# Performance work log

Measured on AMD Instinct MI355X. Metric: run time of the kernel, lower is better.

Reference implementation:

```python
import jax, jax.numpy as jnp
import numpy as np

B, S, TV, TT, E, H = 16, 8, 256, 64, 512, 512


def setup_inputs() -> dict:
    key = jax.random.key(0)
    ks = jax.random.split(key, 24)
    sc = 0.02
    p = lambda k, shape: jax.random.normal(k, shape, jnp.float32) * sc
    inp = {
        'vid_feats': jax.random.normal(ks[0], (B, S, TV, 2 * E), jnp.float32),
        'text_feats': jax.random.normal(ks[1], (B, S, TT, E), jnp.float32),
        'segment_labels': jax.random.randint(ks[2], (B, S), 0, 6),
        # bidirectional LSTM params for video encoder (input dim 2E)
        'vid_Wx_f': p(ks[3], (2 * E, 4 * H)), 'vid_Wh_f': p(ks[4], (H, 4 * H)), 'vid_b_f': jnp.zeros((4 * H,), jnp.float32),
        'vid_Wx_b': p(ks[5], (2 * E, 4 * H)), 'vid_Wh_b': p(ks[6], (H, 4 * H)), 'vid_b_b': jnp.zeros((4 * H,), jnp.float32),
        # bidirectional LSTM params for text encoder (input dim E)
        'txt_Wx_f': p(ks[7], (E, 4 * H)), 'txt_Wh_f': p(ks[8], (H, 4 * H)), 'txt_b_f': jnp.zeros((4 * H,), jnp.float32),
        'txt_Wx_b': p(ks[9], (E, 4 * H)), 'txt_Wh_b': p(ks[10], (H, 4 * H)), 'txt_b_b': jnp.zeros((4 * H,), jnp.float32),
        # state_query MLP: Linear(4H,H) -> ReLU -> (Dropout eval) -> Linear(H,1)
        'sq_W1': p(ks[11], (4 * H, H)), 'sq_b1': jnp.zeros((H,), jnp.float32),
        'sq_W2': p(ks[12], (H, 1)), 'sq_b2': jnp.zeros((1,), jnp.float32),
        # relation_query MLP
        'rq_W1': p(ks[13], (4 * H, H)), 'rq_b1': jnp.zeros((H,), jnp.float32),
        'rq_W2': p(ks[14], (H, 1)), 'rq_b2': jnp.zeros((1,), jnp.float32),
    }
    return inp


def _lstm_last(x, Wx, Wh, b):
    # x: [N, T, D] -> last hidden state [N, H]; gate order i,f,g,o (torch convention)
    xg = jnp.einsum('ntd,dg->ntg', x, Wx) + b  # precompute input projections
    h0 = jnp.zeros((x.shape[0], Wh.shape[0]), x.dtype)

    def step(carry, xt):
        h, c = carry
        i, f, g, o = jnp.split(xt + h @ Wh, 4, axis=-1)
        c = jax.nn.sigmoid(f) * c + jax.nn.sigmoid(i) * jnp.tanh(g)
        h = jax.nn.sigmoid(o) * jnp.tanh(c)
        return (h, c), None

    (h, _), _ = jax.lax.scan(step, (h0, h0), jnp.swapaxes(xg, 0, 1))
    return h


def _bilstm(x, Wxf, Whf, bf, Wxb, Whb, bb):
    # final hidden of fwd dir + final hidden of bwd dir (run on reversed seq)
    hf = _lstm_last(x, Wxf, Whf, bf)
    hb = _lstm_last(x[:, ::-1], Wxb, Whb, bb)
    return jnp.concatenate([hf, hb], axis=-1)  # [N, 2H]


def reference(vid_feats, text_feats,
              vid_Wx_f, vid_Wh_f, vid_b_f, vid_Wx_b, vid_Wh_b, vid_b_b,
              txt_Wx_f, txt_Wh_f, txt_b_f, txt_Wx_b, txt_Wh_b, txt_b_b,
              sq_W1, sq_b1, sq_W2, sq_b2, rq_W1, rq_b1, rq_W2, rq_b2,
              segment_labels):
    b, s = vid_feats.shape[0], vid_feats.shape[1]
    vh = _bilstm(vid_feats.reshape(b * s, vid_feats.shape[2], vid_feats.shape[3]),
                 vid_Wx_f, vid_Wh_f, vid_b_f, vid_Wx_b, vid_Wh_b, vid_b_b)  # [B*S, 2H]
    th = _bilstm(text_feats.reshape(b * s, text_feats.shape[2], text_feats.shape[3]),
                 txt_Wx_f, txt_Wh_f, txt_b_f, txt_Wx_b, txt_Wh_b, txt_b_b)  # [B*S, 2H]
    feats = jnp.concatenate([vh, th], axis=-1).reshape(b, s, -1)  # [B, S, 4H]

    def mlp(W1, b1, W2, b2):
        h = jax.nn.relu(feats @ W1 + b1)  # Dropout is identity in eval mode
        return (h @ W2 + b2)[..., 0]      # [B, S]

    state_score = mlp(sq_W1, sq_b1, sq_W2, sq_b2)
    rel_score = mlp(rq_W1, rq_b1, rq_W2, rq_b2)
    # labels <= 3 -> state_query, labels in {4,5} -> relation_query
    sel = jnp.where(segment_labels <= 3, state_score, rel_score)  # [B, S]
    return jax.nn.sigmoid(sel.mean(axis=1))  # [B]
```

## Files before the change

kernel.cpp:

```cpp
#include <hip/hip_runtime.h>
#include <hip/hip_bf16.h>

typedef __bf16 bf16_t;
typedef __bf16 bf16x8 __attribute__((ext_vector_type(8)));
typedef __bf16 bf16x4 __attribute__((ext_vector_type(4)));
typedef float f32x4 __attribute__((ext_vector_type(4)));
typedef unsigned int u32x4 __attribute__((ext_vector_type(4)));

#define DEVI static __device__ __forceinline__

DEVI f32x4 mfma16(bf16x8 a, bf16x8 b, f32x4 c) {
  return __builtin_amdgcn_mfma_f32_16x16x32_bf16(a, b, c, 0, 0, 0);
}

DEVI float sigf(float x) { return 1.f / (1.f + __expf(-x)); }
DEVI float tanh_fast(float x) { return 2.f / (1.f + __expf(-2.f * x)) - 1.f; }

DEVI void prep_one(const float* __restrict__ src, bf16_t* __restrict__ dst,
                   int K, int N, int gid) {
  int l = gid & 63;
  int fi = gid >> 6;
  int NT = N >> 4;
  int nt = fi % NT;
  int kc = fi / NT;
  int row0 = kc * 32 + (l >> 4) * 8;
  int col = nt * 16 + (l & 15);
  bf16x8 v;
#pragma unroll
  for (int j = 0; j < 8; ++j) v[j] = (bf16_t)src[(size_t)(row0 + j) * N + col];
  *(bf16x8*)(dst + (size_t)gid * 8) = v;
}

__global__ __launch_bounds__(256) void k_prep_all(
    const float* s0, bf16_t* d0, const float* s1, bf16_t* d1,
    const float* s2, bf16_t* d2, const float* s3, bf16_t* d3,
    const float* s4, bf16_t* d4, const float* s5, bf16_t* d5,
    const float* s6, bf16_t* d6, const float* s7, bf16_t* d7,
    const float* s8, bf16_t* d8, const float* s9, bf16_t* d9) {
  int b = blockIdx.x;
  if (b < 1024)       prep_one(s0, d0, 1024, 2048, (b - 0)    * 256 + threadIdx.x);
  else if (b < 2048)  prep_one(s1, d1, 1024, 2048, (b - 1024) * 256 + threadIdx.x);
  else if (b < 2560)  prep_one(s2, d2, 512, 2048,  (b - 2048) * 256 + threadIdx.x);
  else if (b < 3072)  prep_one(s3, d3, 512, 2048,  (b - 2560) * 256 + threadIdx.x);
  else if (b < 3584)  prep_one(s4, d4, 512, 2048,  (b - 3072) * 256 + threadIdx.x);
  else if (b < 4096)  prep_one(s5, d5, 512, 2048,  (b - 3584) * 256 + threadIdx.x);
  else if (b < 4608)  prep_one(s6, d6, 512, 2048,  (b - 4096) * 256 + threadIdx.x);
  else if (b < 5120)  prep_one(s7, d7, 512, 2048,  (b - 4608) * 256 + threadIdx.x);
  else if (b < 5632)  prep_one(s8, d8, 2048, 512,  (b - 5120) * 256 + threadIdx.x);
  else                prep_one(s9, d9, 2048, 512,  (b - 5632) * 256 + threadIdx.x);
}

__global__ __launch_bounds__(256) void k_cvt(const float* __restrict__ src,
                                             bf16_t* __restrict__ dst, int n8) {
  int stride = gridDim.x * 256;
  for (int i = blockIdx.x * 256 + threadIdx.x; i < n8; i += stride) {
    const float4* p = (const float4*)(src + (size_t)i * 8);
    float4 u = p[0], v = p[1];
    bf16x8 o;
    o[0] = (bf16_t)u.x; o[1] = (bf16_t)u.y; o[2] = (bf16_t)u.z; o[3] = (bf16_t)u.w;
    o[4] = (bf16_t)v.x; o[5] = (bf16_t)v.y; o[6] = (bf16_t)v.z; o[7] = (bf16_t)v.w;
    *(bf16x8*)(dst + (size_t)i * 8) = o;
  }
}

template <int KDIM>
__global__ __launch_bounds__(256) void k_proj(const bf16_t* __restrict__ x, int T,
                                              int dir,
                                              const bf16_t* __restrict__ Wsw,
                                              const float* __restrict__ bias,
                                              bf16_t* __restrict__ xg) {
  int chunk = blockIdx.x & 7;
  int t = blockIdx.x >> 3;
  int tt = dir ? (T - 1 - t) : t;
  int tid = threadIdx.x;
  int l = tid & 63, w = tid >> 6;
  int rl = l & 15, lh = l >> 4;
  int m0 = chunk * 16 + w * 4;
  f32x4 acc[4][8];
#pragma unroll
  for (int mi = 0; mi < 4; ++mi)
#pragma unroll
    for (int n = 0; n < 8; ++n) acc[mi][n] = f32x4{0.f, 0.f, 0.f, 0.f};

  for (int kc = 0; kc < KDIM / 32; ++kc) {
    bf16x8 aw[4];
#pragma unroll
    for (int mi = 0; mi < 4; ++mi)
      aw[mi] = *(const bf16x8*)(Wsw + ((size_t)(kc * 128 + m0 + mi) * 64 + l) * 8);
    bf16x8 xb[8];
#pragma unroll
    for (int n = 0; n < 8; ++n) {
      int chain = n * 16 + rl;
      xb[n] = *(const bf16x8*)(x + ((size_t)chain * T + tt) * KDIM + kc * 32 + lh * 8);
    }
#pragma unroll
    for (int mi = 0; mi < 4; ++mi)
#pragma unroll
      for (int n = 0; n < 8; ++n) acc[mi][n] = mfma16(aw[mi], xb[n], acc[mi][n]);
  }

#pragma unroll
  for (int mi = 0; mi < 4; ++mi) {
    int m = m0 + mi;
    float bv[4];
#pragma unroll
    for (int r = 0; r < 4; ++r) bv[r] = bias[m * 16 + lh * 4 + r];
#pragma unroll
    for (int n = 0; n < 8; ++n) {
      bf16x4 ov;
#pragma unroll
      for (int r = 0; r < 4; ++r) ov[r] = (bf16_t)(acc[mi][n][r] + bv[r]);
      *(bf16x4*)(xg + (((size_t)t * 128 + m) * 8 + n) * 256 + l * 4) = ov;
    }
  }
}

__global__ __launch_bounds__(256, 1) void k_rnn(
    const bf16_t* __restrict__ xg_vid, const bf16_t* __restrict__ xg_txt,
    const bf16_t* __restrict__ Wh_vid, const bf16_t* __restrict__ Wh_txt,
    bf16_t* __restrict__ hbuf, int* __restrict__ flags,
    bf16_t* __restrict__ feats) {
  int bid = blockIdx.x;
  int g = bid >> 4;
  int wgi = bid & 15;
  int species = g >> 2, dir = (g >> 1) & 1, half = g & 1;
  int tid = threadIdx.x;
  int w = tid >> 6, l = tid & 63;
  int slot = wgi * 4 + w;
  int jt = slot >> 1;
  int pp = slot & 1;
  int rl = l & 15, lh = l >> 4;
  int jb = jt * 16 + lh * 4;

  int NT = species ? 64 : 256;
  const bf16_t* xg = (species ? xg_txt : xg_vid) + (size_t)dir * NT * (128 * 2048);
  const bf16_t* Wh = (species ? Wh_txt : Wh_vid) + (size_t)dir * (512 * 2048);
  bf16_t* hb = hbuf + (size_t)g * 2 * 32768;
  int* flg = flags + g * 256;
  int colbase = species * 1024 + dir * 512;

  bf16x8 Bw[16][4];
#pragma unroll
  for (int kc = 0; kc < 16; ++kc)
#pragma unroll
    for (int gg = 0; gg < 4; ++gg)
      Bw[kc][gg] = *(const bf16x8*)(Wh + ((size_t)(kc * 128 + gg * 32 + jt) * 64 + l) * 8);

  int kc_w = jt >> 1;
  int l_w = ((jt & 1) * 2 + (lh >> 1)) * 16 + rl;
  int e_w = (lh & 1) * 4;

  float c[2][4];
#pragma unroll
  for (int nn = 0; nn < 2; ++nn)
#pragma unroll
    for (int r = 0; r < 4; ++r) c[nn][r] = 0.f;

  for (int s = 0; s < NT; ++s) {
    bf16x4 xv[4][2];
#pragma unroll
    for (int gg = 0; gg < 4; ++gg)
#pragma unroll
      for (int nn = 0; nn < 2; ++nn)
        xv[gg][nn] = *(const bf16x4*)(
            xg + (((size_t)s * 128 + gg * 32 + jt) * 8 + half * 4 + pp * 2 + nn) * 256 +
            l * 4);

    f32x4 acc[4][2];
#pragma unroll
    for (int gg = 0; gg < 4; ++gg)
#pragma unroll
      for (int nn = 0; nn < 2; ++nn)
        acc[gg][nn] = f32x4{(float)xv[gg][nn][0], (float)xv[gg][nn][1],
                            (float)xv[gg][nn][2], (float)xv[gg][nn][3]};

    if (s > 0) {
      const int* fl = flg + (s - 1);
      while (__hip_atomic_load(fl, __ATOMIC_RELAXED, __HIP_MEMORY_SCOPE_AGENT) < 16)
        __builtin_amdgcn_s_sleep(1);
      asm volatile("" ::: "memory");

      const bf16_t* hcur = hb + (size_t)(s & 1) * 32768;
      u32x4 hf[2][16];
#pragma unroll
      for (int nn = 0; nn < 2; ++nn) {
        int ct = pp * 2 + nn;
#pragma unroll
        for (int kc = 0; kc < 16; ++kc) {
          const bf16_t* hp = hcur + ((size_t)(kc * 4 + ct) * 64 + l) * 8;
          asm volatile("global_load_dwordx4 %0, %1, off sc1"
                       : "=v"(hf[nn][kc]) : "v"(hp) : "memory");
        }
      }
      asm volatile("s_waitcnt vmcnt(0)" ::: "memory");
      __builtin_amdgcn_sched_barrier(0);
#pragma unroll
      for (int kc = 0; kc < 16; ++kc)
#pragma unroll
        for (int gg = 0; gg < 4; ++gg)
#pragma unroll
          for (int nn = 0; nn < 2; ++nn)
            acc[gg][nn] = mfma16(Bw[kc][gg], __builtin_bit_cast(bf16x8, hf[nn][kc]),
                                 acc[gg][nn]);
    }

    bf16_t* hnext = hb + (size_t)((s + 1) & 1) * 32768;
#pragma unroll
    for (int nn = 0; nn < 2; ++nn) {
      int ct = pp * 2 + nn;
      int chain = ct * 16 + rl;
      bf16x4 hv;
#pragma unroll
      for (int r = 0; r < 4; ++r) {
        float iv = acc[0][nn][r], fv = acc[1][nn][r];
        float gv = acc[2][nn][r], ov = acc[3][nn][r];
        float cn = sigf(fv) * c[nn][r] + sigf(iv) * tanh_fast(gv);
        c[nn][r] = cn;
        hv[r] = (bf16_t)(sigf(ov) * tanh_fast(cn));
      }
      __hip_atomic_store(
          (unsigned long long*)(hnext + ((size_t)(kc_w * 4 + ct) * 64 + l_w) * 8 + e_w),
          __builtin_bit_cast(unsigned long long, hv),
          __ATOMIC_RELAXED, __HIP_MEMORY_SCOPE_AGENT);
      if (s == NT - 1)
        *(bf16x4*)(feats + (size_t)(half * 64 + chain) * 2048 + colbase + jb) = hv;
    }

    __syncthreads();
    if (tid == 0)
      __hip_atomic_fetch_add(flg + s, 1, __ATOMIC_RELAXED, __HIP_MEMORY_SCOPE_AGENT);
  }
}

__global__ __launch_bounds__(256) void k_mlp(const bf16_t* __restrict__ feats,
                                             const bf16_t* __restrict__ W1sw,
                                             const float* __restrict__ sqb1,
                                             const float* __restrict__ rqb1,
                                             float* __restrict__ h1) {
  int mlp = blockIdx.x >> 3, chunk = blockIdx.x & 7;
  const bf16_t* Wsw = W1sw + (size_t)mlp * (2048 * 512);
  const float* b1 = mlp ? rqb1 : sqb1;
  int tid = threadIdx.x;
  int l = tid & 63, w = tid >> 6;
  int rl = l & 15, kl = (l >> 4) * 8;
  f32x4 acc[2][4];
#pragma unroll
  for (int mt = 0; mt < 2; ++mt)
#pragma unroll
    for (int nt = 0; nt < 4; ++nt) acc[mt][nt] = f32x4{0.f, 0.f, 0.f, 0.f};

  for (int kc = 0; kc < 64; ++kc) {
    bf16x8 a[2];
#pragma unroll
    for (int mt = 0; mt < 2; ++mt) {
      int row = w * 32 + mt * 16 + rl;
      a[mt] = *(const bf16x8*)(feats + (size_t)row * 2048 + kc * 32 + kl);
    }
#pragma unroll
    for (int nt = 0; nt < 4; ++nt) {
      int nt_g = chunk * 4 + nt;
      bf16x8 b = *(const bf16x8*)(Wsw + ((size_t)(kc * 32 + nt_g) * 64 + l) * 8);
#pragma unroll
      for (int mt = 0; mt < 2; ++mt) acc[mt][nt] = mfma16(a[mt], b, acc[mt][nt]);
    }
  }

#pragma unroll
  for (int mt = 0; mt < 2; ++mt)
#pragma unroll
    for (int nt = 0; nt < 4; ++nt) {
      int col = (chunk * 4 + nt) * 16 + rl;
      float bv = b1[col];
#pragma unroll
      for (int r = 0; r < 4; ++r) {
        int row = w * 32 + mt * 16 + (l >> 4) * 4 + r;
        float v = acc[mt][nt][r] + bv;
        h1[(size_t)mlp * (128 * 512) + (size_t)row * 512 + col] = v > 0.f ? v : 0.f;
      }
    }
}

__global__ __launch_bounds__(256) void k_final(const float* __restrict__ h1,
                                               const float* __restrict__ sqW2,
                                               const float* __restrict__ sqb2,
                                               const float* __restrict__ rqW2,
                                               const float* __restrict__ rqb2,
                                               const int* __restrict__ labels,
                                               float* __restrict__ out) {
  __shared__ float sc[128][2];
  int tid = threadIdx.x;
  int row = tid >> 1, m = tid & 1;
  const float* hp = h1 + ((size_t)m * 128 + row) * 512;
  const float* w2 = m ? rqW2 : sqW2;
  float s = m ? *rqb2 : *sqb2;
  for (int k = 0; k < 512; ++k) s += hp[k] * w2[k];
  sc[row][m] = s;
  __syncthreads();
  if (tid < 16) {
    float acc = 0.f;
    for (int i = 0; i < 8; ++i) {
      int r = tid * 8 + i;
      acc += (labels[r] <= 3) ? sc[r][0] : sc[r][1];
    }
    acc *= (1.f / 8.f);
    out[tid] = 1.f / (1.f + __expf(-acc));
  }
}

extern "C" void kernel_launch(void* const* d_in, const int* in_sizes, int n_in,
                              void* d_out, int out_size, void* d_ws, size_t ws_size,
                              hipStream_t stream) {
  const float* vid  = (const float*)d_in[0];
  const float* txt  = (const float*)d_in[1];
  const int* labels = (const int*)d_in[2];
  const float* vWxf = (const float*)d_in[3];
  const float* vWhf = (const float*)d_in[4];
  const float* vbf  = (const float*)d_in[5];
  const float* vWxb = (const float*)d_in[6];
  const float* vWhb = (const float*)d_in[7];
  const float* vbb  = (const float*)d_in[8];
  const float* tWxf = (const float*)d_in[9];
  const float* tWhf = (const float*)d_in[10];
  const float* tbf  = (const float*)d_in[11];
  const float* tWxb = (const float*)d_in[12];
  const float* tWhb = (const float*)d_in[13];
  const float* tbb  = (const float*)d_in[14];
  const float* sqW1 = (const float*)d_in[15];
  const float* sqb1 = (const float*)d_in[16];
  const float* sqW2 = (const float*)d_in[17];
  const float* sqb2 = (const float*)d_in[18];
  const float* rqW1 = (const float*)d_in[19];
  const float* rqb1 = (const float*)d_in[20];
  const float* rqW2 = (const float*)d_in[21];
  const float* rqb2 = (const float*)d_in[22];

  char* p = (char*)d_ws;
  auto alloc = [&](size_t bytes) {
    char* r = p;
    p += (bytes + 255) & ~(size_t)255;
    return r;
  };
  bf16_t* vWxf_sw = (bf16_t*)alloc((size_t)1024 * 2048 * 2);
  bf16_t* vWxb_sw = (bf16_t*)alloc((size_t)1024 * 2048 * 2);
  bf16_t* vWh_sw  = (bf16_t*)alloc((size_t)2 * 512 * 2048 * 2);
  bf16_t* tWxf_sw = (bf16_t*)alloc((size_t)512 * 2048 * 2);
  bf16_t* tWxb_sw = (bf16_t*)alloc((size_t)512 * 2048 * 2);
  bf16_t* tWh_sw  = (bf16_t*)alloc((size_t)2 * 512 * 2048 * 2);
  bf16_t* W1_sw   = (bf16_t*)alloc((size_t)2 * 2048 * 512 * 2);
  bf16_t* xg_vid  = (bf16_t*)alloc((size_t)2 * 256 * 128 * 2048 * 2);
  bf16_t* xg_txt  = (bf16_t*)alloc((size_t)2 * 64 * 128 * 2048 * 2);
  bf16_t* xbf_vid = (bf16_t*)alloc((size_t)128 * 256 * 1024 * 2);
  bf16_t* xbf_txt = (bf16_t*)alloc((size_t)128 * 64 * 512 * 2);
  bf16_t* hbuf    = (bf16_t*)alloc((size_t)8 * 2 * 32768 * 2);
  int*    flags   = (int*)alloc((size_t)8 * 256 * 4);
  bf16_t* feats   = (bf16_t*)alloc((size_t)128 * 2048 * 2);
  float*  h1      = (float*)alloc((size_t)2 * 128 * 512 * 4);
  (void)ws_size; (void)in_sizes; (void)n_in; (void)out_size;

  k_prep_all<<<6144, 256, 0, stream>>>(
      vWxf, vWxf_sw, vWxb, vWxb_sw, vWhf, vWh_sw,
      vWhb, vWh_sw + (size_t)512 * 2048, tWxf, tWxf_sw, tWxb, tWxb_sw,
      tWhf, tWh_sw, tWhb, tWh_sw + (size_t)512 * 2048,
      sqW1, W1_sw, rqW1, W1_sw + (size_t)2048 * 512);

  k_cvt<<<2048, 256, 0, stream>>>(vid, xbf_vid, 128 * 256 * 1024 / 8);
  k_cvt<<<512, 256, 0, stream>>>(txt, xbf_txt, 128 * 64 * 512 / 8);

  hipMemsetAsync(flags, 0, (size_t)8 * 256 * 4, stream);

  size_t xgv_dir = (size_t)256 * 128 * 2048;
  size_t xgt_dir = (size_t)64 * 128 * 2048;
  k_proj<1024><<<256 * 8, 256, 0, stream>>>(xbf_vid, 256, 0, vWxf_sw, vbf, xg_vid);
  k_proj<1024><<<256 * 8, 256, 0, stream>>>(xbf_vid, 256, 1, vWxb_sw, vbb, xg_vid + xgv_dir);
  k_proj<512><<<64 * 8, 256, 0, stream>>>(xbf_txt, 64, 0, tWxf_sw, tbf, xg_txt);
  k_proj<512><<<64 * 8, 256, 0, stream>>>(xbf_txt, 64, 1, tWxb_sw, tbb, xg_txt + xgt_dir);

  k_rnn<<<128, 256, 0, stream>>>(xg_vid, xg_txt, vWh_sw, tWh_sw, hbuf, flags, feats);

  k_mlp<<<16, 256, 0, stream>>>(feats, W1_sw, sqb1, rqb1, h1);
  k_final<<<1, 256, 0, stream>>>(h1, sqW2, sqb2, rqW2, rqb2, labels, (float*)d_out);
}
```

Before: 2.019 ms.

## Fuse input projection into recurrent kernel with per-timestep flag pipelining

Merges the fp32→bf16 conversion, the input-projection GEMMs and the LSTM recurrence into one persistent launch. 128 producer blocks compute input gates timestep by timestep and publish per-timestep counters, while 128 recurrent blocks spin on those counters alongside their existing h-exchange flags. This lets the recurrence, which is latency-bound, overlap with the projection work, and it removes the separate conversion pass and its bf16 staging buffer. The risks are that all 256 blocks must be co-resident to avoid deadlock, and that producer blocks now share the GPU with the recurrent ones, so the projection runs at lower throughput.

```diff
diff --git a/kernel.cpp b/kernel.cpp
--- a/kernel.cpp
+++ b/kernel.cpp
@@ -6,6 +6,7 @@
 typedef __bf16 bf16x4 __attribute__((ext_vector_type(4)));
 typedef float f32x4 __attribute__((ext_vector_type(4)));
 typedef unsigned int u32x4 __attribute__((ext_vector_type(4)));
+typedef unsigned int u32x2 __attribute__((ext_vector_type(2)));
 
 #define DEVI static __device__ __forceinline__
 
@@ -50,86 +51,103 @@
   else                prep_one(s9, d9, 2048, 512,  (b - 5632) * 256 + threadIdx.x);
 }
 
-__global__ __launch_bounds__(256) void k_cvt(const float* __restrict__ src,
-                                             bf16_t* __restrict__ dst, int n8) {
-  int stride = gridDim.x * 256;
-  for (int i = blockIdx.x * 256 + threadIdx.x; i < n8; i += stride) {
-    const float4* p = (const float4*)(src + (size_t)i * 8);
-    float4 u = p[0], v = p[1];
-    bf16x8 o;
-    o[0] = (bf16_t)u.x; o[1] = (bf16_t)u.y; o[2] = (bf16_t)u.z; o[3] = (bf16_t)u.w;
-    o[4] = (bf16_t)v.x; o[5] = (bf16_t)v.y; o[6] = (bf16_t)v.z; o[7] = (bf16_t)v.w;
-    *(bf16x8*)(dst + (size_t)i * 8) = o;
-  }
-}
-
-template <int KDIM>
-__global__ __launch_bounds__(256) void k_proj(const bf16_t* __restrict__ x, int T,
-                                              int dir,
-                                              const bf16_t* __restrict__ Wsw,
-                                              const float* __restrict__ bias,
-                                              bf16_t* __restrict__ xg) {
-  int chunk = blockIdx.x & 7;
-  int t = blockIdx.x >> 3;
-  int tt = dir ? (T - 1 - t) : t;
-  int tid = threadIdx.x;
-  int l = tid & 63, w = tid >> 6;
-  int rl = l & 15, lh = l >> 4;
-  int m0 = chunk * 16 + w * 4;
-  f32x4 acc[4][8];
-#pragma unroll
-  for (int mi = 0; mi < 4; ++mi)
-#pragma unroll
-    for (int n = 0; n < 8; ++n) acc[mi][n] = f32x4{0.f, 0.f, 0.f, 0.f};
-
-  for (int kc = 0; kc < KDIM / 32; ++kc) {
-    bf16x8 aw[4];
-#pragma unroll
-    for (int mi = 0; mi < 4; ++mi)
-      aw[mi] = *(const bf16x8*)(Wsw + ((size_t)(kc * 128 + m0 + mi) * 64 + l) * 8);
-    bf16x8 xb[8];
-#pragma unroll
-    for (int n = 0; n < 8; ++n) {
-      int chain = n * 16 + rl;
-      xb[n] = *(const bf16x8*)(x + ((size_t)chain * T + tt) * KDIM + kc * 32 + lh * 8);
-    }
-#pragma unroll
-    for (int mi = 0; mi < 4; ++mi)
-#pragma unroll
-      for (int n = 0; n < 8; ++n) acc[mi][n] = mfma16(aw[mi], xb[n], acc[mi][n]);
-  }
-
-#pragma unroll
-  for (int mi = 0; mi < 4; ++mi) {
-    int m = m0 + mi;
-    float bv[4];
-#pragma unroll
-    for (int r = 0; r < 4; ++r) bv[r] = bias[m * 16 + lh * 4 + r];
-#pragma unroll
-    for (int n = 0; n < 8; ++n) {
-      bf16x4 ov;
-#pragma unroll
-      for (int r = 0; r < 4; ++r) ov[r] = (bf16_t)(acc[mi][n][r] + bv[r]);
-      *(bf16x4*)(xg + (((size_t)t * 128 + m) * 8 + n) * 256 + l * 4) = ov;
-    }
-  }
-}
-
-__global__ __launch_bounds__(256, 1) void k_rnn(
-    const bf16_t* __restrict__ xg_vid, const bf16_t* __restrict__ xg_txt,
+__global__ __launch_bounds__(256, 1) void k_fused(
+    const float* __restrict__ vid, const float* __restrict__ txt,
+    const bf16_t* __restrict__ vWxf_sw, const bf16_t* __restrict__ vWxb_sw,
+    const float* __restrict__ vbf, const float* __restrict__ vbb,
+    const bf16_t* __restrict__ tWxf_sw, const bf16_t* __restrict__ tWxb_sw,
+    const float* __restrict__ tbf, const float* __restrict__ tbb,
     const bf16_t* __restrict__ Wh_vid, const bf16_t* __restrict__ Wh_txt,
-    bf16_t* __restrict__ hbuf, int* __restrict__ flags,
+    bf16_t* __restrict__ xg_vid, bf16_t* __restrict__ xg_txt,
+    bf16_t* __restrict__ hbuf, int* __restrict__ flags, int* __restrict__ xgf,
     bf16_t* __restrict__ feats) {
   int bid = blockIdx.x;
-  int g = bid >> 4;
-  int wgi = bid & 15;
-  int species = g >> 2, dir = (g >> 1) & 1, half = g & 1;
   int tid = threadIdx.x;
   int w = tid >> 6, l = tid & 63;
+  int rl = l & 15, lh = l >> 4;
+
+  if (bid < 128) {
+    for (int i = bid; i < 5120; i += 128) {
+      int t, sd, chunk;
+      if (i < 2048) {
+        t = i >> 5; int r = i & 31; sd = r >> 3; chunk = r & 7;
+      } else {
+        int j = i - 2048; t = 64 + (j >> 4); int r = j & 15; sd = r >> 3; chunk = r & 7;
+      }
+      int species = sd >> 1, dirp = sd & 1;
+      int T = species ? 64 : 256;
+      int KD32 = species ? 16 : 32;
+      const float* x = species ? txt : vid;
+      const bf16_t* Wsw = species ? (dirp ? tWxb_sw : tWxf_sw)
+                                  : (dirp ? vWxb_sw : vWxf_sw);
+      const float* bias = species ? (dirp ? tbb : tbf) : (dirp ? vbb : vbf);
+      bf16_t* xg = species ? (xg_txt + (size_t)dirp * 64 * (128 * 2048))
+                           : (xg_vid + (size_t)dirp * 256 * (128 * 2048));
+      int tt = dirp ? (T - 1 - t) : t;
+      int KDIM = KD32 * 32;
+      int m0 = chunk * 16 + w * 4;
+
+      f32x4 acc[4][8];
+#pragma unroll
+      for (int mi = 0; mi < 4; ++mi)
+#pragma unroll
+        for (int n = 0; n < 8; ++n) acc[mi][n] = f32x4{0.f, 0.f, 0.f, 0.f};
+
+      for (int kc = 0; kc < KD32; ++kc) {
+        bf16x8 aw[4];
+#pragma unroll
+        for (int mi = 0; mi < 4; ++mi)
+          aw[mi] = *(const bf16x8*)(Wsw + ((size_t)(kc * 128 + m0 + mi) * 64 + l) * 8);
+        bf16x8 xb[8];
+#pragma unroll
+        for (int n = 0; n < 8; ++n) {
+          int chain = n * 16 + rl;
+          const float* p = x + ((size_t)chain * T + tt) * KDIM + kc * 32 + lh * 8;
+          float4 u = *(const float4*)p;
+          float4 v2 = *(const float4*)(p + 4);
+          bf16x8 bv;
+          bv[0] = (bf16_t)u.x; bv[1] = (bf16_t)u.y; bv[2] = (bf16_t)u.z; bv[3] = (bf16_t)u.w;
+          bv[4] = (bf16_t)v2.x; bv[5] = (bf16_t)v2.y; bv[6] = (bf16_t)v2.z; bv[7] = (bf16_t)v2.w;
+          xb[n] = bv;
+        }
+#pragma unroll
+        for (int mi = 0; mi < 4; ++mi)
+#pragma unroll
+          for (int n = 0; n < 8; ++n) acc[mi][n] = mfma16(aw[mi], xb[n], acc[mi][n]);
+      }
+
+#pragma unroll
+      for (int mi = 0; mi < 4; ++mi) {
+        int m = m0 + mi;
+        float bv[4];
+#pragma unroll
+        for (int r = 0; r < 4; ++r) bv[r] = bias[m * 16 + lh * 4 + r];
+#pragma unroll
+        for (int n = 0; n < 8; ++n) {
+          bf16x4 ov;
+#pragma unroll
+          for (int r = 0; r < 4; ++r) ov[r] = (bf16_t)(acc[mi][n][r] + bv[r]);
+          __hip_atomic_store(
+              (unsigned long long*)(xg + (((size_t)t * 128 + m) * 8 + n) * 256 + l * 4),
+              __builtin_bit_cast(unsigned long long, ov),
+              __ATOMIC_RELAXED, __HIP_MEMORY_SCOPE_AGENT);
+        }
+      }
+      __syncthreads();
+      if (tid == 0)
+        __hip_atomic_fetch_add(xgf + sd * 256 + t, 1, __ATOMIC_RELAXED,
+                               __HIP_MEMORY_SCOPE_AGENT);
+    }
+    return;
+  }
+
+  int rb = bid - 128;
+  int g = rb >> 4;
+  int wgi = rb & 15;
+  int species = g >> 2, dir = (g >> 1) & 1, half = g & 1;
   int slot = wgi * 4 + w;
   int jt = slot >> 1;
   int pp = slot & 1;
-  int rl = l & 15, lh = l >> 4;
   int jb = jt * 16 + lh * 4;
 
   int NT = species ? 64 : 256;
@@ -137,6 +155,7 @@
   const bf16_t* Wh = (species ? Wh_txt : Wh_vid) + (size_t)dir * (512 * 2048);
   bf16_t* hb = hbuf + (size_t)g * 2 * 32768;
   int* flg = flags + g * 256;
+  const int* xfl0 = xgf + (species * 2 + dir) * 256;
   int colbase = species * 1024 + dir * 512;
 
   bf16x8 Bw[16][4];
@@ -157,31 +176,34 @@
     for (int r = 0; r < 4; ++r) c[nn][r] = 0.f;
 
   for (int s = 0; s < NT; ++s) {
-    bf16x4 xv[4][2];
+    {
+      const int* xfl = xfl0 + s;
+      const int* fl = flg + (s > 0 ? s - 1 : 0);
+      for (;;) {
+        int a = __hip_atomic_load(xfl, __ATOMIC_RELAXED, __HIP_MEMORY_SCOPE_AGENT);
+        int b = (s > 0)
+                    ? __hip_atomic_load(fl, __ATOMIC_RELAXED, __HIP_MEMORY_SCOPE_AGENT)
+                    : 16;
+        if (a >= 8 && b >= 16) break;
+        __builtin_amdgcn_s_sleep(1);
+      }
+      asm volatile("" ::: "memory");
+    }
+
+    u32x2 xr[4][2];
 #pragma unroll
     for (int gg = 0; gg < 4; ++gg)
 #pragma unroll
-      for (int nn = 0; nn < 2; ++nn)
-        xv[gg][nn] = *(const bf16x4*)(
+      for (int nn = 0; nn < 2; ++nn) {
+        const bf16_t* xp =
             xg + (((size_t)s * 128 + gg * 32 + jt) * 8 + half * 4 + pp * 2 + nn) * 256 +
-            l * 4);
-
-    f32x4 acc[4][2];
-#pragma unroll
-    for (int gg = 0; gg < 4; ++gg)
-#pragma unroll
-      for (int nn = 0; nn < 2; ++nn)
-        acc[gg][nn] = f32x4{(float)xv[gg][nn][0], (float)xv[gg][nn][1],
-                            (float)xv[gg][nn][2], (float)xv[gg][nn][3]};
-
+            l * 4;
+        asm volatile("global_load_dwordx2 %0, %1, off sc1"
+                     : "=v"(xr[gg][nn]) : "v"(xp) : "memory");
+      }
+    u32x4 hf[2][16];
     if (s > 0) {
-      const int* fl = flg + (s - 1);
-      while (__hip_atomic_load(fl, __ATOMIC_RELAXED, __HIP_MEMORY_SCOPE_AGENT) < 16)
-        __builtin_amdgcn_s_sleep(1);
-      asm volatile("" ::: "memory");
-
       const bf16_t* hcur = hb + (size_t)(s & 1) * 32768;
-      u32x4 hf[2][16];
 #pragma unroll
       for (int nn = 0; nn < 2; ++nn) {
         int ct = pp * 2 + nn;
@@ -192,8 +214,20 @@
                        : "=v"(hf[nn][kc]) : "v"(hp) : "memory");
         }
       }
-      asm volatile("s_waitcnt vmcnt(0)" ::: "memory");
-      __builtin_amdgcn_sched_barrier(0);
+    }
+    asm volatile("s_waitcnt vmcnt(0)" ::: "memory");
+    __builtin_amdgcn_sched_barrier(0);
+
+    f32x4 acc[4][2];
+#pragma unroll
+    for (int gg = 0; gg < 4; ++gg)
+#pragma unroll
+      for (int nn = 0; nn < 2; ++nn) {
+        bf16x4 xv = __builtin_bit_cast(bf16x4, xr[gg][nn]);
+        acc[gg][nn] = f32x4{(float)xv[0], (float)xv[1], (float)xv[2], (float)xv[3]};
+      }
+
+    if (s > 0) {
 #pragma unroll
       for (int kc = 0; kc < 16; ++kc)
 #pragma unroll
@@ -349,10 +383,9 @@
   bf16_t* W1_sw   = (bf16_t*)alloc((size_t)2 * 2048 * 512 * 2);
   bf16_t* xg_vid  = (bf16_t*)alloc((size_t)2 * 256 * 128 * 2048 * 2);
   bf16_t* xg_txt  = (bf16_t*)alloc((size_t)2 * 64 * 128 * 2048 * 2);
-  bf16_t* xbf_vid = (bf16_t*)alloc((size_t)128 * 256 * 1024 * 2);
-  bf16_t* xbf_txt = (bf16_t*)alloc((size_t)128 * 64 * 512 * 2);
   bf16_t* hbuf    = (bf16_t*)alloc((size_t)8 * 2 * 32768 * 2);
   int*    flags   = (int*)alloc((size_t)8 * 256 * 4);
+  int*    xgf     = (int*)alloc((size_t)4 * 256 * 4);
   bf16_t* feats   = (bf16_t*)alloc((size_t)128 * 2048 * 2);
   float*  h1      = (float*)alloc((size_t)2 * 128 * 512 * 4);
   (void)ws_size; (void)in_sizes; (void)n_in; (void)out_size;
@@ -363,19 +396,11 @@
       tWhf, tWh_sw, tWhb, tWh_sw + (size_t)512 * 2048,
       sqW1, W1_sw, rqW1, W1_sw + (size_t)2048 * 512);
 
-  k_cvt<<<2048, 256, 0, stream>>>(vid, xbf_vid, 128 * 256 * 1024 / 8);
-  k_cvt<<<512, 256, 0, stream>>>(txt, xbf_txt, 128 * 64 * 512 / 8);
-
-  hipMemsetAsync(flags, 0, (size_t)8 * 256 * 4, stream);
-
-  size_t xgv_dir = (size_t)256 * 128 * 2048;
-  size_t xgt_dir = (size_t)64 * 128 * 2048;
-  k_proj<1024><<<256 * 8, 256, 0, stream>>>(xbf_vid, 256, 0, vWxf_sw, vbf, xg_vid);
-  k_proj<1024><<<256 * 8, 256, 0, stream>>>(xbf_vid, 256, 1, vWxb_sw, vbb, xg_vid + xgv_dir);
-  k_proj<512><<<64 * 8, 256, 0, stream>>>(xbf_txt, 64, 0, tWxf_sw, tbf, xg_txt);
-  k_proj<512><<<64 * 8, 256, 0, stream>>>(xbf_txt, 64, 1, tWxb_sw, tbb, xg_txt + xgt_dir);
-
-  k_rnn<<<128, 256, 0, stream>>>(xg_vid, xg_txt, vWh_sw, tWh_sw, hbuf, flags, feats);
+  hipMemsetAsync(flags, 0, (size_t)8 * 256 * 4 + (size_t)4 * 256 * 4, stream);
+
+  k_fused<<<256, 256, 0, stream>>>(
+      vid, txt, vWxf_sw, vWxb_sw, vbf, vbb, tWxf_sw, tWxb_sw, tbf, tbb,
+      vWh_sw, tWh_sw, xg_vid, xg_txt, hbuf, flags, xgf, feats);
 
   k_mlp<<<16, 256, 0, stream>>>(feats, W1_sw, sqb1, rqb1, h1);
   k_final<<<1, 256, 0, stream>>>(h1, sqW2, sqb2, rqW2, rqb2, labels, (float*)d_out);
```

Result: slower. 2.746 ms (+36.0%).
